# Optimization experiments

Hardware: AMD Instinct MI355X
Metric: run time of the kernel (lower is better)

## Reference

```python
import jax, jax.numpy as jnp
import numpy as np

EMBED_DIM = 1024
NUM_HEAD = 16
HEAD_DIM = EMBED_DIM // NUM_HEAD


def _linear_params(key, in_dim, out_dim):
    kw, kb = jax.random.split(key)
    bound = 1.0 / np.sqrt(in_dim)
    W = jax.random.uniform(kw, (out_dim, in_dim), minval=-bound, maxval=bound, dtype=jnp.float32)
    b = jax.random.uniform(kb, (out_dim,), minval=-bound, maxval=bound, dtype=jnp.float32)
    return W, b


def setup_inputs() -> dict:
    key = jax.random.key(0)
    ks = jax.random.split(key, 7)
    N, S, E = 2, 2048, EMBED_DIM
    k = jax.random.normal(ks[0], (N, S, E), dtype=jnp.float32)
    q = jax.random.normal(ks[1], (N, S, E), dtype=jnp.float32)
    v = jax.random.normal(ks[2], (N, S, E), dtype=jnp.float32)
    Wk, bk = _linear_params(ks[3], E, E)
    Wq, bq = _linear_params(ks[4], E, E)
    Wv, bv = _linear_params(ks[5], E, E)
    Wo, bo = _linear_params(ks[6], E, E)
    return {"key": k, "query": q, "value": v,
            "Wk": Wk, "bk": bk, "Wq": Wq, "bq": bq,
            "Wv": Wv, "bv": bv, "Wo": Wo, "bo": bo}


def reference(key, query, value, Wk, bk, Wq, bq, Wv, bv, Wo, bo):
    N, S_in, E = key.shape
    S_out = query.shape[1]
    H, D = NUM_HEAD, HEAD_DIM
    # projections (torch Linear: x @ W.T + b), split heads -> [N, H, S, D]
    k = (key @ Wk.T + bk).reshape(N, S_in, H, D).transpose(0, 2, 1, 3)
    q = (query @ Wq.T + bq).reshape(N, S_out, H, D).transpose(0, 2, 1, 3)
    v = (value @ Wv.T + bv).reshape(N, S_in, H, D).transpose(0, 2, 1, 3)
    # unfused attention: full [N,H,S_out,S_in] score matrix, scale, softmax
    weight = jnp.einsum("nhqd,nhkd->nhqk", q, k) / jnp.sqrt(jnp.float32(D))
    weight = jax.nn.softmax(weight, axis=-1)
    attn = jnp.einsum("nhqk,nhkd->nhqd", weight, v)  # [N,H,S_out,D]
    attn = attn.transpose(0, 2, 1, 3).reshape(N, S_out, E)
    return attn @ Wo.T + bo
```

## Files before the change

### kernel.cpp

```cpp
#include <hip/hip_runtime.h>

constexpr int E  = 1024;
constexpr int NH = 16;
constexpr int HD = 64;
constexpr int S  = 2048;
constexpr int NB = 2;
constexpr int M  = NB * S;

typedef unsigned short u16;
typedef _Float16 f16;
typedef __attribute__((ext_vector_type(8))) _Float16 h8v;
typedef __attribute__((ext_vector_type(2))) __fp16 hp2v;
typedef __attribute__((ext_vector_type(4))) float f4v;

__device__ __forceinline__ f4v mfmaH(h8v a, h8v b, f4v c) {
    return __builtin_amdgcn_mfma_f32_16x16x32_f16(a, b, c, 0, 0, 0);
}
__device__ __forceinline__ u16 f16bits(float x) {
    union { f16 h; u16 u; } t; t.h = (f16)x; return t.u;
}
__device__ __forceinline__ unsigned pkrtz(float a, float b) {
    union { hp2v h; unsigned u; } t;
    t.h = __builtin_amdgcn_cvt_pkrtz(a, b);
    return t.u;
}
typedef const __attribute__((address_space(1))) void gvoid;
typedef __attribute__((address_space(3))) void lvoid;
__device__ __forceinline__ void load_lds16(const u16* g, u16* l) {
    __builtin_amdgcn_global_load_lds((gvoid*)g, (lvoid*)l, 16, 0, 0);
}

__global__ __launch_bounds__(256)
void cvt_f16(const float* __restrict__ q, const float* __restrict__ k,
             const float* __restrict__ v,
             const float* __restrict__ wq, const float* __restrict__ wk,
             const float* __restrict__ wv, const float* __restrict__ wo,
             u16* __restrict__ out)
{
    const size_t ME = (size_t)M * E, EE = (size_t)E * E;
    const int z = blockIdx.y;
    const float* src = (z == 0) ? q : (z == 1) ? k : (z == 2) ? v
                     : (z == 3) ? wq : (z == 4) ? wk : (z == 5) ? wv : wo;
    const size_t len = (z < 3) ? ME : EE;
    u16* dst = out + ((z < 3) ? (size_t)z * ME : 3 * ME + (size_t)(z - 3) * EE);
    for (size_t i = ((size_t)blockIdx.x * 256 + threadIdx.x) * 8; i < len;
         i += (size_t)gridDim.x * 256 * 8) {
        float4 a = *reinterpret_cast<const float4*>(src + i);
        float4 b = *reinterpret_cast<const float4*>(src + i + 4);
        h8v o;
        o[0] = (f16)a.x; o[1] = (f16)a.y; o[2] = (f16)a.z; o[3] = (f16)a.w;
        o[4] = (f16)b.x; o[5] = (f16)b.y; o[6] = (f16)b.z; o[7] = (f16)b.w;
        *reinterpret_cast<h8v*>(dst + i) = o;
    }
}

__device__ __forceinline__ void gemm16_core(const u16* __restrict__ A,
                                            const u16* __restrict__ W,
                                            int bm, int bn, u16* lds, f4v acc[4][4])
{
    const int tid  = threadIdx.x;
    const int lane = tid & 63;
    const int wid  = tid >> 6;
    const int g = lane >> 4, c = lane & 15;
    const int wr = wid >> 1, wc = wid & 1;
    const int lrow = lane >> 3;
    const int lslot = lane & 7;
    const int sslot = lslot ^ lrow;

    for (int k0 = 0; k0 < E; k0 += 64) {
        #pragma unroll
        for (int i = 0; i < 4; ++i) {
            int rbase = wid * 32 + i * 8;
            load_lds16(A + (size_t)(bm + rbase + lrow) * E + k0 + (sslot << 3),
                       &lds[rbase * 64]);
            load_lds16(W + (size_t)(bn + rbase + lrow) * E + k0 + (sslot << 3),
                       &lds[8192 + rbase * 64]);
        }
        __syncthreads();

        h8v a[4][2];
        #pragma unroll
        for (int mf = 0; mf < 4; ++mf) {
            int row = wr * 64 + mf * 16 + c;
            #pragma unroll
            for (int ks = 0; ks < 2; ++ks)
                a[mf][ks] = *reinterpret_cast<h8v*>(
                    &lds[row * 64 + ((((ks << 2) | g) ^ (c & 7)) << 3)]);
        }
        #pragma unroll
        for (int nf = 0; nf < 4; ++nf) {
            int row = wc * 64 + nf * 16 + c;
            #pragma unroll
            for (int ks = 0; ks < 2; ++ks) {
                h8v b = *reinterpret_cast<h8v*>(
                    &lds[8192 + row * 64 + ((((ks << 2) | g) ^ (c & 7)) << 3)]);
                #pragma unroll
                for (int mf = 0; mf < 4; ++mf)
                    acc[mf][nf] = mfmaH(a[mf][ks], b, acc[mf][nf]);
            }
        }
        __syncthreads();
    }
}

__global__ __launch_bounds__(256, 3)
void qkv_gemm(const u16* __restrict__ qf, const u16* __restrict__ kf,
              const u16* __restrict__ vf,
              const u16* __restrict__ wqf, const u16* __restrict__ wkf,
              const u16* __restrict__ wvf,
              const float* __restrict__ bq, const float* __restrict__ bk,
              const float* __restrict__ bv,
              u16* __restrict__ Qattn, u16* __restrict__ KV, float scaleQ)
{
    __shared__ __align__(16) u16 lds[16384];
    const int z = blockIdx.z;
    const u16* A = (z == 0) ? qf : (z == 1) ? kf : vf;
    const u16* W = (z == 0) ? wqf : (z == 1) ? wkf : wvf;
    const float* bias = (z == 0) ? bq : (z == 1) ? bk : bv;
    const float scl = (z == 0) ? scaleQ : 1.0f;
    const int bm = blockIdx.x * 128, bn = blockIdx.y * 128;

    f4v acc[4][4];
    #pragma unroll
    for (int a = 0; a < 4; ++a)
        #pragma unroll
        for (int b = 0; b < 4; ++b) acc[a][b] = (f4v){0.f, 0.f, 0.f, 0.f};

    gemm16_core(A, W, bm, bn, lds, acc);

    const int lane = threadIdx.x & 63;
    const int g = lane >> 4, c = lane & 15;
    const int wid = threadIdx.x >> 6;
    const int wr = wid >> 1, wc = wid & 1;
    float bcol[4];
    #pragma unroll
    for (int nf = 0; nf < 4; ++nf) bcol[nf] = bias[bn + wc * 64 + nf * 16 + c];

    #pragma unroll
    for (int mf = 0; mf < 4; ++mf)
        #pragma unroll
        for (int r = 0; r < 4; ++r) {
            int m  = bm + wr * 64 + mf * 16 + g * 4 + r;
            int nb = m >> 11, sp = m & (S - 1);
            #pragma unroll
            for (int nf = 0; nf < 4; ++nf) {
                int ncol = bn + wc * 64 + nf * 16 + c;
                int h = ncol >> 6, d = ncol & 63;
                int bh_ = nb * NH + h;
                u16 hb = f16bits((acc[mf][nf][r] + bcol[nf]) * scl);
                if (z == 0) {
                    Qattn[((size_t)bh_ * S + sp) * HD + d] = hb;
                } else if (z == 1) {
                    int t = sp >> 6, kk = (sp >> 4) & 3, cc = sp & 15;
                    int ds = d >> 5, gg = (d >> 3) & 3, j = d & 7;
                    KV[((size_t)bh_ * 32 + t) * 8192 +
                       ((size_t)((kk * 2 + ds) * 64 + gg * 16 + cc)) * 8 + j] = hb;
                } else {
                    int t = sp >> 6, rem = sp & 63;
                    int s2 = rem >> 5, bb = (rem >> 4) & 1, gg = (rem >> 2) & 3, a2 = rem & 3;
                    int j = 4 * bb + a2;
                    int df = d >> 4, cc = d & 15;
                    KV[((size_t)bh_ * 32 + t) * 8192 + 4096 +
                       ((size_t)((df * 2 + s2) * 64 + gg * 16 + cc)) * 8 + j] = hb;
                }
            }
        }
}

__global__ __launch_bounds__(256, 3)
void out_gemm(const u16* __restrict__ A, const u16* __restrict__ W,
              const float* __restrict__ bias, float* __restrict__ C)
{
    __shared__ __align__(16) u16 lds[16384];
    const int bm = blockIdx.x * 128, bn = blockIdx.y * 128;
    f4v acc[4][4];
    #pragma unroll
    for (int a = 0; a < 4; ++a)
        #pragma unroll
        for (int b = 0; b < 4; ++b) acc[a][b] = (f4v){0.f, 0.f, 0.f, 0.f};

    gemm16_core(A, W, bm, bn, lds, acc);

    const int lane = threadIdx.x & 63;
    const int g = lane >> 4, c = lane & 15;
    const int wid = threadIdx.x >> 6;
    const int wr = wid >> 1, wc = wid & 1;
    float bcol[4];
    #pragma unroll
    for (int nf = 0; nf < 4; ++nf) bcol[nf] = bias[bn + wc * 64 + nf * 16 + c];

    #pragma unroll
    for (int mf = 0; mf < 4; ++mf)
        #pragma unroll
        for (int r = 0; r < 4; ++r) {
            int m = bm + wr * 64 + mf * 16 + g * 4 + r;
            float* crow = &C[(size_t)m * E + bn + wc * 64];
            #pragma unroll
            for (int nf = 0; nf < 4; ++nf)
                crow[nf * 16 + c] = acc[mf][nf][r] + bcol[nf];
        }
}

__global__ __launch_bounds__(256, 4)
void attn_mfma(const u16* __restrict__ Qf, const u16* __restrict__ KV,
               u16* __restrict__ Out)
{
    __shared__ __align__(16) u16 lds[16384];
    const int tid  = threadIdx.x;
    const int lane = tid & 63;
    const int wid  = tid >> 6;
    const int g = lane >> 4, c = lane & 15;
    const int dlin = blockIdx.x;
    const int idx  = dlin >> 3;
    const int bh = (dlin & 7) * 4 + (idx >> 5);
    const int qc = idx & 31;
    const int n = bh >> 4, h = bh & 15;
    const int q0 = qc * 64 + wid * 16;
    const u16* kvb = KV + (size_t)bh * 32 * 8192;
    const f4v zero4 = {0.f, 0.f, 0.f, 0.f};

    h8v Qb[2];
    #pragma unroll
    for (int ds = 0; ds < 2; ++ds)
        Qb[ds] = *reinterpret_cast<const h8v*>(
            &Qf[((size_t)bh * S + q0 + c) * HD + ds * 32 + g * 8]);

    h8v ones;
    #pragma unroll
    for (int i = 0; i < 8; ++i) ones[i] = (f16)1.0f;

    f4v oacc[4];
    #pragma unroll
    for (int df = 0; df < 4; ++df) oacc[df] = zero4;
    f4v lacc = zero4;

    {
        const u16* src = kvb + wid * 2048 + lane * 8;
        u16* dst = &lds[wid * 2048];
        #pragma unroll
        for (int i = 0; i < 4; ++i) load_lds16(src + i * 512, dst + i * 512);
    }
    __syncthreads();

    int cur = 0;
    for (int t = 0; t < 32; ++t) {
        if (t < 31) {
            const u16* src = kvb + (size_t)(t + 1) * 8192 + wid * 2048 + lane * 8;
            u16* dst = &lds[(cur ^ 1) * 8192 + wid * 2048];
            #pragma unroll
            for (int i = 0; i < 4; ++i) load_lds16(src + i * 512, dst + i * 512);
        }
        const u16* Bt = &lds[cur * 8192];

        f4v sc[4];
        #pragma unroll
        for (int kf = 0; kf < 4; ++kf) sc[kf] = zero4;
        __builtin_amdgcn_s_setprio(1);
        #pragma unroll
        for (int kf = 0; kf < 4; ++kf) {
            #pragma unroll
            for (int ds = 0; ds < 2; ++ds) {
                h8v kh = *reinterpret_cast<const h8v*>(
                    &Bt[((size_t)((kf * 2 + ds) * 64 + lane)) * 8]);
                sc[kf] = mfmaH(kh, Qb[ds], sc[kf]);
            }
        }
        __builtin_amdgcn_s_setprio(0);

        unsigned pkh[4][2];
        #pragma unroll
        for (int kf = 0; kf < 4; ++kf) {
            #pragma unroll
            for (int r = 0; r < 4; ++r) sc[kf][r] = exp2f(sc[kf][r]);
            pkh[kf][0] = pkrtz(sc[kf][0], sc[kf][1]);
            pkh[kf][1] = pkrtz(sc[kf][2], sc[kf][3]);
        }

        h8v pah[2];
        #pragma unroll
        for (int s2 = 0; s2 < 2; ++s2) {
            union { h8v v; unsigned u[4]; } th;
            th.u[0] = pkh[2 * s2][0];     th.u[1] = pkh[2 * s2][1];
            th.u[2] = pkh[2 * s2 + 1][0]; th.u[3] = pkh[2 * s2 + 1][1];
            pah[s2] = th.v;
        }

        __builtin_amdgcn_s_setprio(1);
        lacc = mfmaH(pah[0], ones, lacc);
        lacc = mfmaH(pah[1], ones, lacc);
        #pragma unroll
        for (int df = 0; df < 4; ++df) {
            #pragma unroll
            for (int s2 = 0; s2 < 2; ++s2) {
                h8v vh = *reinterpret_cast<const h8v*>(
                    &Bt[4096 + ((size_t)((df * 2 + s2) * 64 + lane)) * 8]);
                oacc[df] = mfmaH(pah[s2], vh, oacc[df]);
            }
        }
        __builtin_amdgcn_s_setprio(0);

        __syncthreads();
        cur ^= 1;
    }

    #pragma unroll
    for (int r = 0; r < 4; ++r) {
        float linv = 1.0f / lacc[r];
        int q = q0 + g * 4 + r;
        size_t ob = ((size_t)n * S + q) * E + h * HD;
        #pragma unroll
        for (int df = 0; df < 4; ++df)
            Out[ob + df * 16 + c] = f16bits(oacc[df][r] * linv);
    }
}

extern "C" void kernel_launch(void* const* d_in, const int* in_sizes, int n_in,
                              void* d_out, int out_size, void* d_ws, size_t ws_size,
                              hipStream_t stream)
{
    const float* key   = (const float*)d_in[0];
    const float* query = (const float*)d_in[1];
    const float* value = (const float*)d_in[2];
    const float* Wk    = (const float*)d_in[3];
    const float* bk    = (const float*)d_in[4];
    const float* Wq    = (const float*)d_in[5];
    const float* bq    = (const float*)d_in[6];
    const float* Wv    = (const float*)d_in[7];
    const float* bv    = (const float*)d_in[8];
    const float* Wo    = (const float*)d_in[9];
    const float* bo    = (const float*)d_in[10];

    const size_t ME = (size_t)M * E, EE = (size_t)E * E;
    u16* ws16  = (u16*)d_ws;
    u16* qf16  = ws16;
    u16* kf16  = ws16 + ME;
    u16* vf16  = ws16 + 2 * ME;
    u16* wqf   = ws16 + 3 * ME;
    u16* wkf   = wqf + EE;
    u16* wvf   = wkf + EE;
    u16* wof   = wvf + EE;
    u16* Qattn = wof + EE;
    u16* KV    = Qattn + ME;
    u16* AoutH = ws16;

    const float SCALE_Q = 0.125f * 1.44269504088896340736f;

    cvt_f16<<<dim3(2048, 7), 256, 0, stream>>>(query, key, value, Wq, Wk, Wv, Wo, ws16);
    qkv_gemm<<<dim3(M / 128, E / 128, 3), 256, 0, stream>>>(
        qf16, kf16, vf16, wqf, wkf, wvf, bq, bk, bv, Qattn, KV, SCALE_Q);
    attn_mfma<<<dim3((S / 64) * NB * NH), 256, 0, stream>>>(Qattn, KV, AoutH);
    out_gemm<<<dim3(M / 128, E / 128), 256, 0, stream>>>(AoutH, wof, bo, (float*)d_out);
}
```

Measured before the change: 127.8 us.

## Prefetch two KV tiles ahead with vmcnt-based waits and hoisted V loads

Restructures the attention inner loop so two KV tiles are prefetched into the double-buffered LDS before the loop. Each iteration waits only for the older tile using s_waitcnt vmcnt(4) plus a raw barrier, instead of a full __syncthreads after each tile. V fragments are now read from LDS before the QK MFMAs so their latency overlaps compute. The aim is to hide global-to-LDS load latency more deeply, at the cost of reliance on manual vmcnt counting, which breaks if the compiler emits other vector memory ops in between.

Result: no change. 127.4 us (-0.3%).

```diff
diff --git a/kernel.cpp b/kernel.cpp
--- a/kernel.cpp
+++ b/kernel.cpp
@@ -239,69 +239,82 @@
         u16* dst = &lds[wid * 2048];
         #pragma unroll
         for (int i = 0; i < 4; ++i) load_lds16(src + i * 512, dst + i * 512);
-    }
-    __syncthreads();
+        src += 8192;
+        dst += 8192;
+        #pragma unroll
+        for (int i = 0; i < 4; ++i) load_lds16(src + i * 512, dst + i * 512);
+    }
 
     int cur = 0;
-    for (int t = 0; t < 32; ++t) {
-        if (t < 31) {
-            const u16* src = kvb + (size_t)(t + 1) * 8192 + wid * 2048 + lane * 8;
-            u16* dst = &lds[(cur ^ 1) * 8192 + wid * 2048];
+    #define ATTN_TILE_BODY(BT)                                                  \
+    {                                                                           \
+        const u16* Bt = (BT);                                                   \
+                                    \
+        h8v vh[4][2];                                                           \
+        _Pragma("unroll")                                                       \
+        for (int df = 0; df < 4; ++df)                                          \
+            _Pragma("unroll")                                                   \
+            for (int s2 = 0; s2 < 2; ++s2)                                      \
+                vh[df][s2] = *reinterpret_cast<const h8v*>(                     \
+                    &Bt[4096 + ((size_t)((df * 2 + s2) * 64 + lane)) * 8]);     \
+        f4v sc[4];                                                              \
+        _Pragma("unroll")                                                       \
+        for (int kf = 0; kf < 4; ++kf) sc[kf] = zero4;                          \
+        __builtin_amdgcn_s_setprio(1);                                          \
+        _Pragma("unroll")                                                       \
+        for (int kf = 0; kf < 4; ++kf) {                                        \
+            _Pragma("unroll")                                                   \
+            for (int ds = 0; ds < 2; ++ds) {                                    \
+                h8v kh = *reinterpret_cast<const h8v*>(                         \
+                    &Bt[((size_t)((kf * 2 + ds) * 64 + lane)) * 8]);            \
+                sc[kf] = mfmaH(kh, Qb[ds], sc[kf]);                             \
+            }                                                                   \
+        }                                                                       \
+        __builtin_amdgcn_s_setprio(0);                                          \
+        unsigned pkh[4][2];                                                     \
+        _Pragma("unroll")                                                       \
+        for (int kf = 0; kf < 4; ++kf) {                                        \
+            _Pragma("unroll")                                                   \
+            for (int r = 0; r < 4; ++r) sc[kf][r] = exp2f(sc[kf][r]);           \
+            pkh[kf][0] = pkrtz(sc[kf][0], sc[kf][1]);                           \
+            pkh[kf][1] = pkrtz(sc[kf][2], sc[kf][3]);                           \
+        }                                                                       \
+        h8v pah[2];                                                             \
+        _Pragma("unroll")                                                       \
+        for (int s2 = 0; s2 < 2; ++s2) {                                        \
+            union { h8v v; unsigned u[4]; } th;                                 \
+            th.u[0] = pkh[2 * s2][0];     th.u[1] = pkh[2 * s2][1];             \
+            th.u[2] = pkh[2 * s2 + 1][0]; th.u[3] = pkh[2 * s2 + 1][1];         \
+            pah[s2] = th.v;                                                     \
+        }                                                                       \
+        __builtin_amdgcn_s_setprio(1);                                          \
+        lacc = mfmaH(pah[0], ones, lacc);                                       \
+        lacc = mfmaH(pah[1], ones, lacc);                                       \
+        _Pragma("unroll")                                                       \
+        for (int df = 0; df < 4; ++df)                                          \
+            _Pragma("unroll")                                                   \
+            for (int s2 = 0; s2 < 2; ++s2)                                      \
+                oacc[df] = mfmaH(pah[s2], vh[df][s2], oacc[df]);                \
+        __builtin_amdgcn_s_setprio(0);                                          \
+    }
+
+    for (int t = 0; t < 31; ++t) {
+        asm volatile("s_waitcnt vmcnt(4)" ::: "memory");
+        __builtin_amdgcn_s_barrier();
+        ATTN_TILE_BODY(&lds[cur * 8192]);
+        __builtin_amdgcn_s_barrier();
+        if (t < 30) {
+            const u16* src = kvb + (size_t)(t + 2) * 8192 + wid * 2048 + lane * 8;
+            u16* dst = &lds[cur * 8192 + wid * 2048];
             #pragma unroll
             for (int i = 0; i < 4; ++i) load_lds16(src + i * 512, dst + i * 512);
         }
-        const u16* Bt = &lds[cur * 8192];
-
-        f4v sc[4];
-        #pragma unroll
-        for (int kf = 0; kf < 4; ++kf) sc[kf] = zero4;
-        __builtin_amdgcn_s_setprio(1);
-        #pragma unroll
-        for (int kf = 0; kf < 4; ++kf) {
-            #pragma unroll
-            for (int ds = 0; ds < 2; ++ds) {
-                h8v kh = *reinterpret_cast<const h8v*>(
-                    &Bt[((size_t)((kf * 2 + ds) * 64 + lane)) * 8]);
-                sc[kf] = mfmaH(kh, Qb[ds], sc[kf]);
-            }
-        }
-        __builtin_amdgcn_s_setprio(0);
-
-        unsigned pkh[4][2];
-        #pragma unroll
-        for (int kf = 0; kf < 4; ++kf) {
-            #pragma unroll
-            for (int r = 0; r < 4; ++r) sc[kf][r] = exp2f(sc[kf][r]);
-            pkh[kf][0] = pkrtz(sc[kf][0], sc[kf][1]);
-            pkh[kf][1] = pkrtz(sc[kf][2], sc[kf][3]);
-        }
-
-        h8v pah[2];
-        #pragma unroll
-        for (int s2 = 0; s2 < 2; ++s2) {
-            union { h8v v; unsigned u[4]; } th;
-            th.u[0] = pkh[2 * s2][0];     th.u[1] = pkh[2 * s2][1];
-            th.u[2] = pkh[2 * s2 + 1][0]; th.u[3] = pkh[2 * s2 + 1][1];
-            pah[s2] = th.v;
-        }
-
-        __builtin_amdgcn_s_setprio(1);
-        lacc = mfmaH(pah[0], ones, lacc);
-        lacc = mfmaH(pah[1], ones, lacc);
-        #pragma unroll
-        for (int df = 0; df < 4; ++df) {
-            #pragma unroll
-            for (int s2 = 0; s2 < 2; ++s2) {
-                h8v vh = *reinterpret_cast<const h8v*>(
-                    &Bt[4096 + ((size_t)((df * 2 + s2) * 64 + lane)) * 8]);
-                oacc[df] = mfmaH(pah[s2], vh, oacc[df]);
-            }
-        }
-        __builtin_amdgcn_s_setprio(0);
-
-        __syncthreads();
         cur ^= 1;
     }
+    asm volatile("s_waitcnt vmcnt(0)" ::: "memory");
+    __builtin_amdgcn_s_barrier();
+    ATTN_TILE_BODY(&lds[cur * 8192]);
+    #undef ATTN_TILE_BODY
 
     #pragma unroll
     for (int r = 0; r < 4; ++r) {
```
